# Kernel tuning notes

Measured on AMD Instinct MI355X. Metric: run time of the kernel, lower is better.

The kernel has to match this reference:

```python
import jax, jax.numpy as jnp
import numpy as np
from numpy.polynomial import Polynomial

EXP_START, EXP_STOP, EXP_N, EXP_DEG = -5.0, 5.0, 1000, 8
INV_START, INV_STOP, INV_N, INV_DEG = 1000.0, 6000.0, 1000, 4


def _ls_fit_coeffs(fn, start, stop, n, deg):
    # least-squares polynomial fit, converted to power basis (matches torch module)
    xs = np.linspace(start, stop, n)
    return Polynomial.fit(xs, fn(xs), deg).convert(kind=Polynomial).coef


def _horner(coeffs, x):
    # coeffs[k] is the coefficient of x**k (power basis); evaluate via Horner
    acc = jnp.full_like(x, coeffs[-1])
    for k in range(coeffs.shape[0] - 2, -1, -1):
        acc = acc * x + coeffs[k]
    return acc


def setup_inputs() -> dict:
    key = jax.random.key(0)
    x = jax.random.normal(key, (16, 2048, 2048), dtype=jnp.float32)
    exp_coeffs = jnp.asarray(_ls_fit_coeffs(np.exp, EXP_START, EXP_STOP, EXP_N, EXP_DEG), dtype=jnp.float32)
    inverse_coeffs = jnp.asarray(_ls_fit_coeffs(lambda t: 1.0 / t, INV_START, INV_STOP, INV_N, INV_DEG), dtype=jnp.float32)
    return {"x": x, "exp_coeffs": exp_coeffs, "inverse_coeffs": inverse_coeffs, "iterations": 3}


def reference(x, exp_coeffs, inverse_coeffs, iterations):
    # CKKS-style softmax: polynomial exp, row-sum, polynomial initial inverse,
    # Newton-Raphson reciprocal refinement, broadcast multiply.
    e = _horner(exp_coeffs, x)                      # [B, S, S] approx exp(x)
    s = jnp.sum(e, axis=-1, keepdims=True)          # [B, S, 1]
    y = _horner(inverse_coeffs, s)                  # initial guess for 1/s
    for _ in range(iterations):                     # Newton: y <- y*(2 - s*y)
        y = y * (2.0 - s * y)
    return e * y
```

## Files before the change

### kernel.cpp

```cpp
#include <hip/hip_runtime.h>


typedef float v4f __attribute__((ext_vector_type(4)));

#define ROWLEN 2048
#define TPB    256
#define ROWS_PER_BLOCK 4

__global__ __launch_bounds__(TPB) void ckks_softmax_kernel(
    const float* __restrict__ x,
    const float* __restrict__ exp_c,
    const float* __restrict__ inv_c,
    const int*   __restrict__ iters_p,
    float* __restrict__ out)
{
    const int lane = threadIdx.x & 63;
    const int wave = threadIdx.x >> 6;
    const int row  = blockIdx.x * ROWS_PER_BLOCK + wave;
    const size_t base = (size_t)row * ROWLEN;

    const v4f* __restrict__ xv = (const v4f*)(x + base);
    v4f*       __restrict__ ov = (v4f*)(out + base);

    const float c0 = exp_c[0], c1 = exp_c[1], c2 = exp_c[2], c3 = exp_c[3],
                c4 = exp_c[4], c5 = exp_c[5], c6 = exp_c[6], c7 = exp_c[7],
                c8 = exp_c[8];
    const float i0 = inv_c[0], i1 = inv_c[1], i2 = inv_c[2], i3 = inv_c[3],
                i4 = inv_c[4];
    const int iters = *iters_p;

    v4f v[8];
    #pragma unroll
    for (int k = 0; k < 8; ++k)
        v[k] = __builtin_nontemporal_load(&xv[lane + 64 * k]);

    auto horner8 = [&](float t) -> float {
        float acc = c8;
        acc = fmaf(acc, t, c7);
        acc = fmaf(acc, t, c6);
        acc = fmaf(acc, t, c5);
        acc = fmaf(acc, t, c4);
        acc = fmaf(acc, t, c3);
        acc = fmaf(acc, t, c2);
        acc = fmaf(acc, t, c1);
        acc = fmaf(acc, t, c0);
        return acc;
    };

    v4f acc4 = {0.0f, 0.0f, 0.0f, 0.0f};
    #pragma unroll
    for (int k = 0; k < 8; ++k) {
        v4f e;
        e.x = horner8(v[k].x);
        e.y = horner8(v[k].y);
        e.z = horner8(v[k].z);
        e.w = horner8(v[k].w);
        v[k] = e;
        acc4 += e;
    }
    float s = (acc4.x + acc4.y) + (acc4.z + acc4.w);

    #pragma unroll
    for (int off = 32; off > 0; off >>= 1)
        s += __shfl_xor(s, off, 64);

    float y = i4;
    y = fmaf(y, s, i3);
    y = fmaf(y, s, i2);
    y = fmaf(y, s, i1);
    y = fmaf(y, s, i0);

    for (int i = 0; i < iters; ++i)
        y = y * (2.0f - s * y);

    #pragma unroll
    for (int k = 0; k < 8; ++k) {
        v4f e = v[k] * y;
        __builtin_nontemporal_store(e, &ov[lane + 64 * k]);
    }
}

extern "C" void kernel_launch(void* const* d_in, const int* in_sizes, int n_in,
                              void* d_out, int out_size, void* d_ws, size_t ws_size,
                              hipStream_t stream) {
    const float* x     = (const float*)d_in[0];
    const float* exp_c = (const float*)d_in[1];
    const float* inv_c = (const float*)d_in[2];
    const int*   iters = (const int*)d_in[3];
    float* out = (float*)d_out;

    const int n_rows = out_size / ROWLEN;
    const int n_blocks = n_rows / ROWS_PER_BLOCK;
    ckks_softmax_kernel<<<n_blocks, TPB, 0, stream>>>(x, exp_c, inv_c, iters, out);
}
```

Before: 424.1 us.

## Process four rows per wave with register double-buffered prefetch of next row

```diff
diff --git a/kernel.cpp b/kernel.cpp
--- a/kernel.cpp
+++ b/kernel.cpp
@@ -3,9 +3,10 @@
 
 typedef float v4f __attribute__((ext_vector_type(4)));
 
-#define ROWLEN 2048
-#define TPB    256
-#define ROWS_PER_BLOCK 4
+#define ROWLEN          2048
+#define TPB             256
+#define WAVES_PER_BLOCK 4
+#define ROWS_PER_WAVE   4
 
 __global__ __launch_bounds__(TPB) void ckks_softmax_kernel(
     const float* __restrict__ x,
@@ -16,11 +17,8 @@
 {
     const int lane = threadIdx.x & 63;
     const int wave = threadIdx.x >> 6;
-    const int row  = blockIdx.x * ROWS_PER_BLOCK + wave;
-    const size_t base = (size_t)row * ROWLEN;
-
-    const v4f* __restrict__ xv = (const v4f*)(x + base);
-    v4f*       __restrict__ ov = (v4f*)(out + base);
+    const size_t gwave = (size_t)blockIdx.x * WAVES_PER_BLOCK + wave;
+    const size_t row0  = gwave * ROWS_PER_WAVE;
 
     const float c0 = exp_c[0], c1 = exp_c[1], c2 = exp_c[2], c3 = exp_c[3],
                 c4 = exp_c[4], c5 = exp_c[5], c6 = exp_c[6], c7 = exp_c[7],
@@ -28,11 +26,6 @@
     const float i0 = inv_c[0], i1 = inv_c[1], i2 = inv_c[2], i3 = inv_c[3],
                 i4 = inv_c[4];
     const int iters = *iters_p;
-
-    v4f v[8];
-    #pragma unroll
-    for (int k = 0; k < 8; ++k)
-        v[k] = __builtin_nontemporal_load(&xv[lane + 64 * k]);
 
     auto horner8 = [&](float t) -> float {
         float acc = c8;
@@ -47,36 +40,63 @@
         return acc;
     };
 
-    v4f acc4 = {0.0f, 0.0f, 0.0f, 0.0f};
-    #pragma unroll
-    for (int k = 0; k < 8; ++k) {
-        v4f e;
-        e.x = horner8(v[k].x);
-        e.y = horner8(v[k].y);
-        e.z = horner8(v[k].z);
-        e.w = horner8(v[k].w);
-        v[k] = e;
-        acc4 += e;
+    v4f cur[8], nxt[8];
+
+    {
+        const v4f* __restrict__ src = (const v4f*)(x + row0 * ROWLEN);
+        #pragma unroll
+        for (int k = 0; k < 8; ++k)
+            cur[k] = src[lane + 64 * k];
     }
-    float s = (acc4.x + acc4.y) + (acc4.z + acc4.w);
 
     #pragma unroll
-    for (int off = 32; off > 0; off >>= 1)
-        s += __shfl_xor(s, off, 64);
+    for (int r = 0; r < ROWS_PER_WAVE; ++r) {
+        if (r + 1 < ROWS_PER_WAVE) {
+            const v4f* __restrict__ srcn =
+                (const v4f*)(x + (row0 + (size_t)(r + 1)) * ROWLEN);
+            #pragma unroll
+            for (int k = 0; k < 8; ++k)
+                nxt[k] = srcn[lane + 64 * k];
+        }
 
-    float y = i4;
-    y = fmaf(y, s, i3);
-    y = fmaf(y, s, i2);
-    y = fmaf(y, s, i1);
-    y = fmaf(y, s, i0);
+        v4f acc4 = {0.0f, 0.0f, 0.0f, 0.0f};
+        #pragma unroll
+        for (int k = 0; k < 8; ++k) {
+            v4f e;
+            e.x = horner8(cur[k].x);
+            e.y = horner8(cur[k].y);
+            e.z = horner8(cur[k].z);
+            e.w = horner8(cur[k].w);
+            cur[k] = e;
+            acc4 += e;
+        }
+        float s = (acc4.x + acc4.y) + (acc4.z + acc4.w);
 
-    for (int i = 0; i < iters; ++i)
-        y = y * (2.0f - s * y);
+        #pragma unroll
+        for (int off = 32; off > 0; off >>= 1)
+            s += __shfl_xor(s, off, 64);
 
-    #pragma unroll
-    for (int k = 0; k < 8; ++k) {
-        v4f e = v[k] * y;
-        __builtin_nontemporal_store(e, &ov[lane + 64 * k]);
+        float y = i4;
+        y = fmaf(y, s, i3);
+        y = fmaf(y, s, i2);
+        y = fmaf(y, s, i1);
+        y = fmaf(y, s, i0);
+
+        for (int i = 0; i < iters; ++i)
+            y = y * (2.0f - s * y);
+
+        v4f* __restrict__ dst = (v4f*)(out + (row0 + (size_t)r) * ROWLEN);
+        #pragma unroll
+        for (int k = 0; k < 8; ++k) {
+            v4f e = cur[k] * y;
+            __builtin_nontemporal_store(e, &dst[lane + 64 * k]);
+        }
+
+        if (r + 1 < ROWS_PER_WAVE) {
+            #pragma unroll
+            for (int k = 0; k < 8; ++k)
+                cur[k] = nxt[k];
+        }
     }
 }
 
@@ -89,7 +109,7 @@
     const int*   iters = (const int*)d_in[3];
     float* out = (float*)d_out;
 
-    const int n_rows = out_size / ROWLEN;
-    const int n_blocks = n_rows / ROWS_PER_BLOCK;
+    const int n_rows   = out_size / ROWLEN;
+    const int n_blocks = n_rows / (WAVES_PER_BLOCK * ROWS_PER_WAVE);
     ckks_softmax_kernel<<<n_blocks, TPB, 0, stream>>>(x, exp_c, inv_c, iters, out);
 }
```

Result: slower. 448.8 us (+5.8%).

## Process four rows per wave with double-buffered register prefetch

Applied to the files above, without the earlier changes.

```diff
diff --git a/kernel.cpp b/kernel.cpp
--- a/kernel.cpp
+++ b/kernel.cpp
@@ -3,9 +3,10 @@
 
 typedef float v4f __attribute__((ext_vector_type(4)));
 
-#define ROWLEN 2048
-#define TPB    256
-#define ROWS_PER_BLOCK 4
+#define ROWLEN          2048
+#define TPB             256
+#define WPB             (TPB / 64)
+#define ROWS_PER_WAVE   4
 
 __global__ __launch_bounds__(TPB) void ckks_softmax_kernel(
     const float* __restrict__ x,
@@ -14,13 +15,9 @@
     const int*   __restrict__ iters_p,
     float* __restrict__ out)
 {
-    const int lane = threadIdx.x & 63;
-    const int wave = threadIdx.x >> 6;
-    const int row  = blockIdx.x * ROWS_PER_BLOCK + wave;
-    const size_t base = (size_t)row * ROWLEN;
-
-    const v4f* __restrict__ xv = (const v4f*)(x + base);
-    v4f*       __restrict__ ov = (v4f*)(out + base);
+    const int lane   = threadIdx.x & 63;
+    const int wid    = blockIdx.x * WPB + (threadIdx.x >> 6);
+    const int nwaves = gridDim.x * WPB;
 
     const float c0 = exp_c[0], c1 = exp_c[1], c2 = exp_c[2], c3 = exp_c[3],
                 c4 = exp_c[4], c5 = exp_c[5], c6 = exp_c[6], c7 = exp_c[7],
@@ -28,11 +25,6 @@
     const float i0 = inv_c[0], i1 = inv_c[1], i2 = inv_c[2], i3 = inv_c[3],
                 i4 = inv_c[4];
     const int iters = *iters_p;
-
-    v4f v[8];
-    #pragma unroll
-    for (int k = 0; k < 8; ++k)
-        v[k] = __builtin_nontemporal_load(&xv[lane + 64 * k]);
 
     auto horner8 = [&](float t) -> float {
         float acc = c8;
@@ -47,37 +39,60 @@
         return acc;
     };
 
-    v4f acc4 = {0.0f, 0.0f, 0.0f, 0.0f};
-    #pragma unroll
-    for (int k = 0; k < 8; ++k) {
-        v4f e;
-        e.x = horner8(v[k].x);
-        e.y = horner8(v[k].y);
-        e.z = horner8(v[k].z);
-        e.w = horner8(v[k].w);
-        v[k] = e;
-        acc4 += e;
-    }
-    float s = (acc4.x + acc4.y) + (acc4.z + acc4.w);
+    auto loadrow = [&](v4f (&buf)[8], int row) {
+        const v4f* __restrict__ src = (const v4f*)(x + (size_t)row * ROWLEN);
+        #pragma unroll
+        for (int k = 0; k < 8; ++k)
+            buf[k] = src[lane + 64 * k];
+    };
 
-    #pragma unroll
-    for (int off = 32; off > 0; off >>= 1)
-        s += __shfl_xor(s, off, 64);
+    auto procrow = [&](v4f (&buf)[8], int row) {
+        v4f acc4 = {0.0f, 0.0f, 0.0f, 0.0f};
+        #pragma unroll
+        for (int k = 0; k < 8; ++k) {
+            v4f e;
+            e.x = horner8(buf[k].x);
+            e.y = horner8(buf[k].y);
+            e.z = horner8(buf[k].z);
+            e.w = horner8(buf[k].w);
+            buf[k] = e;
+            acc4 += e;
+        }
+        float s = (acc4.x + acc4.y) + (acc4.z + acc4.w);
 
-    float y = i4;
-    y = fmaf(y, s, i3);
-    y = fmaf(y, s, i2);
-    y = fmaf(y, s, i1);
-    y = fmaf(y, s, i0);
+        #pragma unroll
+        for (int off = 32; off > 0; off >>= 1)
+            s += __shfl_xor(s, off, 64);
 
-    for (int i = 0; i < iters; ++i)
-        y = y * (2.0f - s * y);
+        float y = i4;
+        y = fmaf(y, s, i3);
+        y = fmaf(y, s, i2);
+        y = fmaf(y, s, i1);
+        y = fmaf(y, s, i0);
 
-    #pragma unroll
-    for (int k = 0; k < 8; ++k) {
-        v4f e = v[k] * y;
-        __builtin_nontemporal_store(e, &ov[lane + 64 * k]);
-    }
+        for (int i = 0; i < iters; ++i)
+            y = y * (2.0f - s * y);
+
+        v4f* __restrict__ dst = (v4f*)(out + (size_t)row * ROWLEN);
+        #pragma unroll
+        for (int k = 0; k < 8; ++k)
+            dst[lane + 64 * k] = buf[k] * y;
+    };
+
+    v4f A[8], B[8];
+    const int r0 = wid;
+    const int r1 = wid + nwaves;
+    const int r2 = wid + 2 * nwaves;
+    const int r3 = wid + 3 * nwaves;
+
+    loadrow(A, r0);
+    loadrow(B, r1);
+    procrow(A, r0);
+    loadrow(A, r2);
+    procrow(B, r1);
+    loadrow(B, r3);
+    procrow(A, r2);
+    procrow(B, r3);
 }
 
 extern "C" void kernel_launch(void* const* d_in, const int* in_sizes, int n_in,
@@ -89,7 +104,7 @@
     const int*   iters = (const int*)d_in[3];
     float* out = (float*)d_out;
 
-    const int n_rows = out_size / ROWLEN;
-    const int n_blocks = n_rows / ROWS_PER_BLOCK;
+    const int n_rows   = out_size / ROWLEN;
+    const int n_blocks = n_rows / (WPB * ROWS_PER_WAVE);
     ckks_softmax_kernel<<<n_blocks, TPB, 0, stream>>>(x, exp_c, inv_c, iters, out);
 }
```

Result: slower. 442.5 us (+4.3%).
